# Kernel optimization log

Hardware: AMD Instinct MI355X
Metric: run time of the kernel (lower is better)

Reference implementation:

```python
import jax, jax.numpy as jnp
import numpy as np

N = 50000
E = 800000
IN_CH = 128
HID = 64
H1 = 4  # heads in gat1
NEG_SLOPE = 0.2


def _gat_layer(x, src, dst, W, a_src, a_dst, bias, heads, ch):
    # x: [N, F_in]; W: [F_in, heads*ch]; a_src/a_dst: [heads, ch]; bias: [heads*ch]
    n = x.shape[0]
    h = (x @ W).reshape(n, heads, ch)                       # [N, H, C]
    alpha_src = jnp.einsum('nhc,hc->nh', h, a_src)          # [N, H]
    alpha_dst = jnp.einsum('nhc,hc->nh', h, a_dst)          # [N, H]
    e = jax.nn.leaky_relu(alpha_src[src] + alpha_dst[dst], NEG_SLOPE)  # [E, H]
    # segment softmax over incoming edges of each destination node
    m = jax.ops.segment_max(e, dst, num_segments=n)         # [N, H]
    ex = jnp.exp(e - m[dst])                                # [E, H]
    denom = jax.ops.segment_sum(ex, dst, num_segments=n)    # [N, H]
    alpha = ex / (denom[dst] + 1e-16)                       # [E, H]
    out = jax.ops.segment_sum(alpha[:, :, None] * h[src], dst, num_segments=n)  # [N, H, C]
    return out.reshape(n, heads * ch) + bias


def setup_inputs() -> dict:
    key = jax.random.key(0)
    ks = jax.random.split(key, 12)
    x = jax.random.normal(ks[0], (N, IN_CH), dtype=jnp.float32)
    edge_index = jax.random.randint(ks[1], (2, E), 0, N, dtype=jnp.int64)
    s1 = 1.0 / np.sqrt(IN_CH)
    s2 = 1.0 / np.sqrt(H1 * HID)
    s3 = 1.0 / np.sqrt(HID)
    return {
        'x': x,
        'edge_index': edge_index,
        'W1': jax.random.uniform(ks[2], (IN_CH, H1 * HID), jnp.float32, -s1, s1),
        'att_src1': jax.random.uniform(ks[3], (H1, HID), jnp.float32, -s1, s1),
        'att_dst1': jax.random.uniform(ks[4], (H1, HID), jnp.float32, -s1, s1),
        'b1': jnp.zeros((H1 * HID,), jnp.float32),
        'W2': jax.random.uniform(ks[5], (H1 * HID, HID), jnp.float32, -s2, s2),
        'att_src2': jax.random.uniform(ks[6], (1, HID), jnp.float32, -s2, s2),
        'att_dst2': jax.random.uniform(ks[7], (1, HID), jnp.float32, -s2, s2),
        'b2': jnp.zeros((HID,), jnp.float32),
        'W_out': jax.random.uniform(ks[8], (HID, 1), jnp.float32, -s3, s3),
        'b_out': jnp.zeros((1,), jnp.float32),
    }


def reference(x, edge_index, W1, att_src1, att_dst1, b1, W2, att_src2, att_dst2, b2, W_out, b_out):
    # add self-loops (PyG GATConv default)
    loops = jnp.arange(N, dtype=edge_index.dtype)
    src = jnp.concatenate([edge_index[0], loops])
    dst = jnp.concatenate([edge_index[1], loops])
    h = jax.nn.relu(_gat_layer(x, src, dst, W1, att_src1, att_dst1, b1, H1, HID))
    h = jax.nn.relu(_gat_layer(h, src, dst, W2, att_src2, att_dst2, b2, 1, HID))
    return (h @ W_out + b_out).squeeze(-1)  # [N]
```

## Files before the change

### kernel.cpp

```cpp
#include <hip/hip_runtime.h>
#include <hip/hip_bf16.h>
#include <math.h>

#define N_NODES 50000
#define N_EDGES 800000
#define EE_TOTAL (N_EDGES + N_NODES)
#define CAP 64

#define GEMM1_BLOCKS ((N_NODES + 63) / 64)
#define SCAT_BLOCKS ((EE_TOTAL + 1023) / 1024)
#define FUSED_BLOCKS (GEMM1_BLOCKS + SCAT_BLOCKS)

typedef __attribute__((ext_vector_type(8))) short bf16x8;
typedef __attribute__((ext_vector_type(4))) float f32x4;

__device__ __forceinline__ float bf2f(unsigned short s) {
  return __uint_as_float((unsigned)s << 16);
}
__device__ __forceinline__ unsigned short f2bf(float f) {
  unsigned u = __float_as_uint(f);
  return (unsigned short)((u + 0x7FFFu + ((u >> 16) & 1u)) >> 16);
}
__device__ __forceinline__ float lrelu(float e) { return e > 0.f ? e : 0.2f * e; }

__global__ void prep_kernel(const float* __restrict__ W1, const float* __restrict__ W2,
                            unsigned short* __restrict__ W1t, unsigned short* __restrict__ W2t,
                            int* __restrict__ counts) {
  int i = blockIdx.x * blockDim.x + threadIdx.x;
  if (i < N_NODES) counts[i] = 0;
  if (i < 256 * 128) W1t[i] = f2bf(W1[(i & 127) * 256 + (i >> 7)]);
  if (i < 64 * 256) W2t[i] = f2bf(W2[(i & 255) * 64 + (i >> 8)]);
}

__device__ __forceinline__ void scatter_body(int sid, int t,
                                             const int* __restrict__ src,
                                             const int* __restrict__ dst,
                                             int* __restrict__ counts,
                                             unsigned short* __restrict__ col) {
  int base = sid * 1024 + t * 4;
  int ss[4], dd[4];
#pragma unroll
  for (int k = 0; k < 4; ++k) {
    int i = base + k;
    if (i < N_EDGES) { ss[k] = src[i]; dd[k] = dst[i]; }
    else if (i < EE_TOTAL) { ss[k] = i - N_EDGES; dd[k] = ss[k]; }
    else { ss[k] = 0; dd[k] = -1; }
  }
#pragma unroll
  for (int k = 0; k < 4; ++k) {
    if (dd[k] >= 0) {
      int pos = atomicAdd(&counts[dd[k]], 1);
      if (pos < CAP) col[(size_t)dd[k] * CAP + pos] = (unsigned short)ss[k];
    }
  }
}

__global__ __launch_bounds__(256) void fused_kernel(const int* __restrict__ src,
                                                    const int* __restrict__ dst,
                                                    int* __restrict__ counts,
                                                    unsigned short* __restrict__ col,
                                                    const float* __restrict__ A,
                                                    const unsigned short* __restrict__ Bt,
                                                    unsigned short* __restrict__ Cb,
                                                    const float* __restrict__ att_s,
                                                    const float* __restrict__ att_d,
                                                    float* __restrict__ as_out,
                                                    float* __restrict__ ad_out) {
  __shared__ unsigned short Bs[256 * 128];
  int b = blockIdx.x;
  int t = threadIdx.x;
  bool is_gemm;
  int id;
  if (b < 2 * GEMM1_BLOCKS) { is_gemm = (b & 1) == 0; id = b >> 1; }
  else { is_gemm = false; id = b - GEMM1_BLOCKS; }

  if (!is_gemm) {
    scatter_body(id, t, src, dst, counts, col);
    return;
  }

  const int M = N_NODES;
  int lane = t & 63, w = t >> 6;
  int row0 = id * 64;
#pragma unroll
  for (int i = 0; i < 16; ++i) {
    int idx = i * 256 + t;
    int n = idx >> 4;
    uint4 v = ((const uint4*)Bt)[idx];
    int byte = (idx * 16) ^ ((n & 7) << 4);
    *(uint4*)((char*)Bs + byte) = v;
  }
  __syncthreads();
  int rl = lane & 15, kg = lane >> 4;
  f32x4 acc[4][4] = {};
  for (int ks = 0; ks < 4; ++ks) {
    bf16x8 af[4], bfr[4];
#pragma unroll
    for (int rb = 0; rb < 4; ++rb) {
      int row = row0 + rb * 16 + rl;
      float4 v0 = make_float4(0.f, 0.f, 0.f, 0.f), v1 = v0;
      if (row < M) {
        const float* p = A + (size_t)row * 128 + ks * 32 + kg * 8;
        v0 = *(const float4*)p;
        v1 = *(const float4*)(p + 4);
      }
      bf16x8 a;
      a[0] = (short)f2bf(v0.x); a[1] = (short)f2bf(v0.y);
      a[2] = (short)f2bf(v0.z); a[3] = (short)f2bf(v0.w);
      a[4] = (short)f2bf(v1.x); a[5] = (short)f2bf(v1.y);
      a[6] = (short)f2bf(v1.z); a[7] = (short)f2bf(v1.w);
      af[rb] = a;
    }
#pragma unroll
    for (int cb = 0; cb < 4; ++cb) {
      int n = w * 64 + cb * 16 + rl;
      int byte = (n * 256 + ks * 64 + kg * 16) ^ ((n & 7) << 4);
      bfr[cb] = *(const bf16x8*)((char*)Bs + byte);
    }
#pragma unroll
    for (int rb = 0; rb < 4; ++rb)
#pragma unroll
      for (int cb = 0; cb < 4; ++cb)
        acc[rb][cb] = __builtin_amdgcn_mfma_f32_16x16x32_bf16(af[rb], bfr[cb], acc[rb][cb], 0, 0, 0);
  }
  float asv[4], adv[4];
#pragma unroll
  for (int cb = 0; cb < 4; ++cb) {
    int c = w * 64 + cb * 16 + rl;
    asv[cb] = att_s[c];
    adv[cb] = att_d[c];
  }
#pragma unroll
  for (int rb = 0; rb < 4; ++rb) {
#pragma unroll
    for (int r = 0; r < 4; ++r) {
      int row = row0 + rb * 16 + kg * 4 + r;
      bool ok = row < M;
      float sp = 0.f, dp = 0.f;
#pragma unroll
      for (int cb = 0; cb < 4; ++cb) {
        float v = acc[rb][cb][r];
        if (ok) Cb[(size_t)row * 256 + w * 64 + cb * 16 + rl] = f2bf(v);
        sp += v * asv[cb];
        dp += v * adv[cb];
      }
#pragma unroll
      for (int off = 1; off < 16; off <<= 1) {
        sp += __shfl_xor(sp, off, 64);
        dp += __shfl_xor(dp, off, 64);
      }
      if (ok && rl == 0) {
        as_out[row * 4 + w] = sp;
        ad_out[row * 4 + w] = dp;
      }
    }
  }
}

__global__ __launch_bounds__(256) void gemm2_kernel(const unsigned short* __restrict__ A,
                                                    const unsigned short* __restrict__ Bt,
                                                    unsigned short* __restrict__ Cb,
                                                    const float* __restrict__ att_s,
                                                    const float* __restrict__ att_d,
                                                    float* __restrict__ as_out,
                                                    float* __restrict__ ad_out) {
  __shared__ unsigned short Bs[64 * 256];
  const int M = N_NODES;
  int t = threadIdx.x;
  int lane = t & 63, w = t >> 6;
  int row0 = blockIdx.x * 64;
#pragma unroll
  for (int i = 0; i < 8; ++i) {
    int idx = i * 256 + t;
    int n = idx >> 5;
    uint4 v = ((const uint4*)Bt)[idx];
    int byte = (idx * 16) ^ ((n & 7) << 4);
    *(uint4*)((char*)Bs + byte) = v;
  }
  __syncthreads();
  int rl = lane & 15, kg = lane >> 4;
  int arow = row0 + w * 16 + rl;
  f32x4 acc[4] = {};
  for (int ks = 0; ks < 8; ++ks) {
    bf16x8 a = {};
    if (arow < M) a = *(const bf16x8*)(A + (size_t)arow * 256 + ks * 32 + kg * 8);
#pragma unroll
    for (int cb = 0; cb < 4; ++cb) {
      int n = cb * 16 + rl;
      int byte = (n * 512 + ks * 64 + kg * 16) ^ ((n & 7) << 4);
      bf16x8 bfrag = *(const bf16x8*)((char*)Bs + byte);
      acc[cb] = __builtin_amdgcn_mfma_f32_16x16x32_bf16(a, bfrag, acc[cb], 0, 0, 0);
    }
  }
  float asv[4], adv[4];
#pragma unroll
  for (int cb = 0; cb < 4; ++cb) {
    int c = cb * 16 + rl;
    asv[cb] = att_s[c];
    adv[cb] = att_d[c];
  }
#pragma unroll
  for (int r = 0; r < 4; ++r) {
    int orow = row0 + w * 16 + kg * 4 + r;
    bool ok = orow < M;
    float sp = 0.f, dp = 0.f;
#pragma unroll
    for (int cb = 0; cb < 4; ++cb) {
      float v = acc[cb][r];
      if (ok) Cb[(size_t)orow * 64 + cb * 16 + rl] = f2bf(v);
      sp += v * asv[cb];
      dp += v * adv[cb];
    }
#pragma unroll
    for (int off = 1; off < 16; off <<= 1) {
      sp += __shfl_xor(sp, off, 64);
      dp += __shfl_xor(dp, off, 64);
    }
    if (ok && rl == 0) {
      as_out[orow] = sp;
      ad_out[orow] = dp;
    }
  }
}

__global__ __launch_bounds__(256) void agg1_kernel(const unsigned short* __restrict__ h1b,
                                                   const float* __restrict__ as,
                                                   const float* __restrict__ ad,
                                                   const int* __restrict__ counts,
                                                   const unsigned short* __restrict__ col,
                                                   const float* __restrict__ b1,
                                                   unsigned short* __restrict__ x2b) {
  __shared__ int s_lds[4][64];
  __shared__ float p_lds[4][64][4];
  int t = threadIdx.x;
  int lane = t & 63, w = t >> 6;
  int node = blockIdx.x * 4 + w;
  if (node >= N_NODES) return;
  int cnt = min(counts[node], CAP);
  const unsigned short* cbase = col + (size_t)node * CAP;
  float4 adn = *(const float4*)(ad + node * 4);
  int half = lane >> 5, sl = lane & 31, hd = sl >> 3;
  int s = node;
  float4 p = make_float4(0.f, 0.f, 0.f, 0.f);
  if (lane < cnt) {
    s = cbase[lane];
    float4 a4 = *(const float4*)(as + s * 4);
    p.x = __expf(lrelu(a4.x + adn.x));
    p.y = __expf(lrelu(a4.y + adn.y));
    p.z = __expf(lrelu(a4.z + adn.z));
    p.w = __expf(lrelu(a4.w + adn.w));
  }
  s_lds[w][lane] = s;
  *(float4*)&p_lds[w][lane][0] = p;
  float4 den = p;
#pragma unroll
  for (int off = 1; off < 64; off <<= 1) {
    den.x += __shfl_xor(den.x, off, 64);
    den.y += __shfl_xor(den.y, off, 64);
    den.z += __shfl_xor(den.z, off, 64);
    den.w += __shfl_xor(den.w, off, 64);
  }
  float acc[8] = {};
  int nq = (cnt + 3) & ~3;
  for (int j = 0; j < nq; j += 4) {
    int e0 = j + half, e1 = j + 2 + half;
    int s0 = s_lds[w][e0], s1 = s_lds[w][e1];
    float p0 = p_lds[w][e0][hd], p1 = p_lds[w][e1][hd];
    bf16x8 v0 = *(const bf16x8*)(h1b + (size_t)s0 * 256 + sl * 8);
    bf16x8 v1 = *(const bf16x8*)(h1b + (size_t)s1 * 256 + sl * 8);
#pragma unroll
    for (int k = 0; k < 8; ++k) {
      acc[k] += p0 * bf2f((unsigned short)v0[k]);
      acc[k] += p1 * bf2f((unsigned short)v1[k]);
    }
  }
#pragma unroll
  for (int k = 0; k < 8; ++k) acc[k] += __shfl_xor(acc[k], 32, 64);
  if (half == 0) {
    float dh = (hd == 0) ? den.x : (hd == 1) ? den.y : (hd == 2) ? den.z : den.w;
    float inv = 1.f / (dh + 1e-16f);
    int ch = sl * 8;
    float4 blo = *(const float4*)(b1 + ch);
    float4 bhi = *(const float4*)(b1 + ch + 4);
    float bb[8] = {blo.x, blo.y, blo.z, blo.w, bhi.x, bhi.y, bhi.z, bhi.w};
    bf16x8 o;
#pragma unroll
    for (int k = 0; k < 8; ++k) o[k] = (short)f2bf(fmaxf(acc[k] * inv + bb[k], 0.f));
    *(bf16x8*)(x2b + (size_t)node * 256 + ch) = o;
  }
}

__global__ __launch_bounds__(256) void agg2_final_kernel(const unsigned short* __restrict__ h2b,
                                                         const float* __restrict__ as,
                                                         const float* __restrict__ ad,
                                                         const int* __restrict__ counts,
                                                         const unsigned short* __restrict__ col,
                                                         const float* __restrict__ b2,
                                                         const float* __restrict__ Wout,
                                                         const float* __restrict__ bout,
                                                         float* __restrict__ out) {
  __shared__ int s_lds[4][64];
  __shared__ float p_lds[4][64];
  int t = threadIdx.x;
  int lane = t & 63, w = t >> 6;
  int node = blockIdx.x * 4 + w;
  if (node >= N_NODES) return;
  int cnt = min(counts[node], CAP);
  const unsigned short* cbase = col + (size_t)node * CAP;
  float adn = ad[node];
  int g = lane >> 4, sl = lane & 15;
  int s = node;
  float p = 0.f;
  if (lane < cnt) {
    s = cbase[lane];
    p = __expf(lrelu(as[s] + adn));
  }
  s_lds[w][lane] = s;
  p_lds[w][lane] = p;
  float den = p;
#pragma unroll
  for (int off = 1; off < 64; off <<= 1) den += __shfl_xor(den, off, 64);
  float acc[4] = {};
  int nq = (cnt + 7) & ~7;
  for (int j = 0; j < nq; j += 8) {
    int e0 = j + g, e1 = j + 4 + g;
    int s0 = s_lds[w][e0], s1 = s_lds[w][e1];
    float p0 = p_lds[w][e0], p1 = p_lds[w][e1];
    ushort4 v0 = *(const ushort4*)(h2b + (size_t)s0 * 64 + sl * 4);
    ushort4 v1 = *(const ushort4*)(h2b + (size_t)s1 * 64 + sl * 4);
    acc[0] += p0 * bf2f(v0.x) + p1 * bf2f(v1.x);
    acc[1] += p0 * bf2f(v0.y) + p1 * bf2f(v1.y);
    acc[2] += p0 * bf2f(v0.z) + p1 * bf2f(v1.z);
    acc[3] += p0 * bf2f(v0.w) + p1 * bf2f(v1.w);
  }
#pragma unroll
  for (int k = 0; k < 4; ++k) {
    acc[k] += __shfl_xor(acc[k], 16, 64);
    acc[k] += __shfl_xor(acc[k], 32, 64);
  }
  float inv = 1.f / (den + 1e-16f);
  int ch = sl * 4;
  float4 b4 = *(const float4*)(b2 + ch);
  float4 w4 = *(const float4*)(Wout + ch);
  float part = fmaxf(acc[0] * inv + b4.x, 0.f) * w4.x +
               fmaxf(acc[1] * inv + b4.y, 0.f) * w4.y +
               fmaxf(acc[2] * inv + b4.z, 0.f) * w4.z +
               fmaxf(acc[3] * inv + b4.w, 0.f) * w4.w;
#pragma unroll
  for (int off = 1; off < 16; off <<= 1) part += __shfl_xor(part, off, 64);
  if (lane == 0) out[node] = part + bout[0];
}

extern "C" void kernel_launch(void* const* d_in, const int* in_sizes, int n_in,
                              void* d_out, int out_size, void* d_ws, size_t ws_size,
                              hipStream_t stream) {
  const float* x    = (const float*)d_in[0];
  const int*   ei   = (const int*)d_in[1];
  const float* W1   = (const float*)d_in[2];
  const float* as1w = (const float*)d_in[3];
  const float* ad1w = (const float*)d_in[4];
  const float* b1   = (const float*)d_in[5];
  const float* W2   = (const float*)d_in[6];
  const float* as2w = (const float*)d_in[7];
  const float* ad2w = (const float*)d_in[8];
  const float* b2   = (const float*)d_in[9];
  const float* Wout = (const float*)d_in[10];
  const float* bout = (const float*)d_in[11];
  float* out = (float*)d_out;

  const int* src = ei;
  const int* dst = ei + N_EDGES;

  char* ws = (char*)d_ws;
  size_t off = 0;
  auto alloc = [&](size_t bytes) -> char* {
    char* p = ws + off;
    off += (bytes + 255) & ~(size_t)255;
    return p;
  };
  int*            counts = (int*)alloc((size_t)N_NODES * 4);
  unsigned short* col    = (unsigned short*)alloc((size_t)N_NODES * CAP * 2);
  unsigned short* W1t    = (unsigned short*)alloc((size_t)256 * 128 * 2);
  unsigned short* W2t    = (unsigned short*)alloc((size_t)64 * 256 * 2);
  unsigned short* x2b    = (unsigned short*)alloc((size_t)N_NODES * 256 * 2);
  unsigned short* hbuf   = (unsigned short*)alloc((size_t)N_NODES * 256 * 2);
  float*          as1    = (float*)alloc((size_t)N_NODES * 4 * 4);
  float*          ad1    = (float*)alloc((size_t)N_NODES * 4 * 4);
  float*          as2    = (float*)alloc((size_t)N_NODES * 4);
  float*          ad2    = (float*)alloc((size_t)N_NODES * 4);

  unsigned short* h1b = hbuf;
  unsigned short* h2b = hbuf;

  const int node_blocks4 = (N_NODES + 3) / 4;
  const int gemm_blocks = (N_NODES + 63) / 64;

  prep_kernel<<<(N_NODES + 255) / 256, 256, 0, stream>>>(W1, W2, W1t, W2t, counts);

  fused_kernel<<<FUSED_BLOCKS, 256, 0, stream>>>(src, dst, counts, col,
                                                 x, W1t, h1b, as1w, ad1w, as1, ad1);

  agg1_kernel<<<node_blocks4, 256, 0, stream>>>(h1b, as1, ad1, counts, col, b1, x2b);

  gemm2_kernel<<<gemm_blocks, 256, 0, stream>>>(x2b, W2t, h2b, as2w, ad2w, as2, ad2);
  agg2_final_kernel<<<node_blocks4, 256, 0, stream>>>(h2b, as2, ad2, counts, col, b2,
                                                      Wout, bout, out);
}
```

Measured before the change: 157.5 us.

## Split layer-1 aggregation per head with half-wave per node and head-interleaved blocks

Rewrites the layer-1 aggregation kernel so that each half-wave (32 lanes) handles one (node, head) pair instead of a full wave handling all four heads of a node. Block indices are interleaved so that consecutive blocks cover different heads of the same node groups, which keeps a head's 128-byte slice of h1 rows hot in cache across those blocks. The aim is to gather only one head's slice per neighbour, with more edges in flight per lane. The cost is that the column indices and attention scores are recomputed once per head, giving four times the index and `as` reads, and the grid is hardcoded to 25000 blocks.

```diff
diff --git a/kernel.cpp b/kernel.cpp
--- a/kernel.cpp
+++ b/kernel.cpp
@@ -10,6 +10,7 @@
 #define GEMM1_BLOCKS ((N_NODES + 63) / 64)
 #define SCAT_BLOCKS ((EE_TOTAL + 1023) / 1024)
 #define FUSED_BLOCKS (GEMM1_BLOCKS + SCAT_BLOCKS)
+#define AGG1_BLOCKS 25000
 
 typedef __attribute__((ext_vector_type(8))) short bf16x8;
 typedef __attribute__((ext_vector_type(4))) float f32x4;
@@ -230,56 +231,57 @@
                                                    const unsigned short* __restrict__ col,
                                                    const float* __restrict__ b1,
                                                    unsigned short* __restrict__ x2b) {
-  __shared__ int s_lds[4][64];
-  __shared__ float p_lds[4][64][4];
+  __shared__ int s_lds[8][64];
+  __shared__ float p_lds[8][64];
+  int bid = blockIdx.x;
+  int head = (bid & 7) >> 1;
+  int idx = (bid >> 3) * 2 + (bid & 1);
   int t = threadIdx.x;
-  int lane = t & 63, w = t >> 6;
-  int node = blockIdx.x * 4 + w;
-  if (node >= N_NODES) return;
+  int hw = t >> 5;
+  int sl = t & 31;
+  int node = idx * 8 + hw;
   int cnt = min(counts[node], CAP);
   const unsigned short* cbase = col + (size_t)node * CAP;
-  float4 adn = *(const float4*)(ad + node * 4);
-  int half = lane >> 5, sl = lane & 31, hd = sl >> 3;
-  int s = node;
-  float4 p = make_float4(0.f, 0.f, 0.f, 0.f);
-  if (lane < cnt) {
-    s = cbase[lane];
-    float4 a4 = *(const float4*)(as + s * 4);
-    p.x = __expf(lrelu(a4.x + adn.x));
-    p.y = __expf(lrelu(a4.y + adn.y));
-    p.z = __expf(lrelu(a4.z + adn.z));
-    p.w = __expf(lrelu(a4.w + adn.w));
-  }
-  s_lds[w][lane] = s;
-  *(float4*)&p_lds[w][lane][0] = p;
-  float4 den = p;
-#pragma unroll
-  for (int off = 1; off < 64; off <<= 1) {
-    den.x += __shfl_xor(den.x, off, 64);
-    den.y += __shfl_xor(den.y, off, 64);
-    den.z += __shfl_xor(den.z, off, 64);
-    den.w += __shfl_xor(den.w, off, 64);
-  }
+  float adn = ad[node * 4 + head];
+  float den = 0.f;
+#pragma unroll
+  for (int c0 = 0; c0 < 64; c0 += 32) {
+    int e = c0 + sl;
+    int s = node;
+    float p = 0.f;
+    if (e < cnt) {
+      s = cbase[e];
+      p = __expf(lrelu(as[s * 4 + head] + adn));
+    }
+    s_lds[hw][e] = s;
+    p_lds[hw][e] = p;
+    den += p;
+  }
+#pragma unroll
+  for (int off = 1; off < 32; off <<= 1) den += __shfl_xor(den, off, 64);
+  int e_off = sl >> 3, cl = sl & 7;
+  const unsigned short* hb = h1b + head * 64 + cl * 8;
   float acc[8] = {};
-  int nq = (cnt + 3) & ~3;
-  for (int j = 0; j < nq; j += 4) {
-    int e0 = j + half, e1 = j + 2 + half;
-    int s0 = s_lds[w][e0], s1 = s_lds[w][e1];
-    float p0 = p_lds[w][e0][hd], p1 = p_lds[w][e1][hd];
-    bf16x8 v0 = *(const bf16x8*)(h1b + (size_t)s0 * 256 + sl * 8);
-    bf16x8 v1 = *(const bf16x8*)(h1b + (size_t)s1 * 256 + sl * 8);
+  int nq = (cnt + 7) & ~7;
+  for (int j = 0; j < nq; j += 8) {
+    int ea = j + e_off, eb = j + 4 + e_off;
+    int sa = s_lds[hw][ea], sb = s_lds[hw][eb];
+    float pa = p_lds[hw][ea], pb = p_lds[hw][eb];
+    bf16x8 va = *(const bf16x8*)(hb + (size_t)sa * 256);
+    bf16x8 vb = *(const bf16x8*)(hb + (size_t)sb * 256);
 #pragma unroll
     for (int k = 0; k < 8; ++k) {
-      acc[k] += p0 * bf2f((unsigned short)v0[k]);
-      acc[k] += p1 * bf2f((unsigned short)v1[k]);
-    }
-  }
-#pragma unroll
-  for (int k = 0; k < 8; ++k) acc[k] += __shfl_xor(acc[k], 32, 64);
-  if (half == 0) {
-    float dh = (hd == 0) ? den.x : (hd == 1) ? den.y : (hd == 2) ? den.z : den.w;
-    float inv = 1.f / (dh + 1e-16f);
-    int ch = sl * 8;
+      acc[k] += pa * bf2f((unsigned short)va[k]) + pb * bf2f((unsigned short)vb[k]);
+    }
+  }
+#pragma unroll
+  for (int k = 0; k < 8; ++k) {
+    acc[k] += __shfl_xor(acc[k], 8, 64);
+    acc[k] += __shfl_xor(acc[k], 16, 64);
+  }
+  if (e_off == 0) {
+    float inv = 1.f / (den + 1e-16f);
+    int ch = head * 64 + cl * 8;
     float4 blo = *(const float4*)(b1 + ch);
     float4 bhi = *(const float4*)(b1 + ch + 4);
     float bb[8] = {blo.x, blo.y, blo.z, blo.w, bhi.x, bhi.y, bhi.z, bhi.w};
@@ -400,7 +402,7 @@
   fused_kernel<<<FUSED_BLOCKS, 256, 0, stream>>>(src, dst, counts, col,
                                                  x, W1t, h1b, as1w, ad1w, as1, ad1);
 
-  agg1_kernel<<<node_blocks4, 256, 0, stream>>>(h1b, as1, ad1, counts, col, b1, x2b);
+  agg1_kernel<<<AGG1_BLOCKS, 256, 0, stream>>>(h1b, as1, ad1, counts, col, b1, x2b);
 
   gemm2_kernel<<<gemm_blocks, 256, 0, stream>>>(x2b, W2t, h2b, as2w, ad2w, as2, ad2);
   agg2_final_kernel<<<node_blocks4, 256, 0, stream>>>(h2b, as2, ad2, counts, col, b2,
```

After: 153.9 us. 2.3% less time.
